# Kernel optimization log

Measured on AMD Instinct MI355X. Metric: run time of the kernel, lower is better.

## Reference

```python
import jax, jax.numpy as jnp
import numpy as np

N_NODES = 50000
N_EDGES = 300000
NODE_DIM = 11
EDGE_DIM = 5
HID = 256
L = 4
G = 1024  # num graphs
BN_EPS = 1e-5


def setup_inputs() -> dict:
    key = jax.random.key(0)
    ks = jax.random.split(key, 24)
    s = 0.05
    inp = {
        "x": jax.random.normal(ks[0], (N_NODES, NODE_DIM), jnp.float32),
        "edge_index": jax.random.randint(ks[1], (2, N_EDGES), 0, N_NODES, jnp.int32),
        "edge_attr": jax.random.normal(ks[2], (N_EDGES, EDGE_DIM), jnp.float32),
        "batch": jnp.sort(jax.random.randint(ks[3], (N_NODES,), 0, G, jnp.int32)),
        # node encoder
        "enc_W": jax.random.normal(ks[4], (NODE_DIM, HID), jnp.float32) * s,
        "enc_b": jnp.zeros((HID,), jnp.float32),
        # per-layer GINE params (stacked over layers)
        "edge_W": jax.random.normal(ks[5], (L, EDGE_DIM, HID), jnp.float32) * s,
        "edge_b": jnp.zeros((L, HID), jnp.float32),
        "mlp_W1": jax.random.normal(ks[6], (L, HID, HID), jnp.float32) * s,
        "mlp_b1": jnp.zeros((L, HID), jnp.float32),
        "mlp_W2": jax.random.normal(ks[7], (L, HID, HID), jnp.float32) * s,
        "mlp_b2": jnp.zeros((L, HID), jnp.float32),
        "bn_g": jnp.ones((L, HID), jnp.float32),
        "bn_b": jnp.zeros((L, HID), jnp.float32),
        # head: 3*HID -> HID -> HID//2 -> 1
        "head_W1": jax.random.normal(ks[8], (3 * HID, HID), jnp.float32) * s,
        "head_b1": jnp.zeros((HID,), jnp.float32),
        "head_W2": jax.random.normal(ks[9], (HID, HID // 2), jnp.float32) * s,
        "head_b2": jnp.zeros((HID // 2,), jnp.float32),
        "head_W3": jax.random.normal(ks[10], (HID // 2, 1), jnp.float32) * s,
        "head_b3": jnp.zeros((1,), jnp.float32),
    }
    return inp


def _forward(x, edge_attr, enc_W, enc_b, edge_W, edge_b, mlp_W1, mlp_b1,
             mlp_W2, mlp_b2, bn_g, bn_b, head_W1, head_b1, head_W2, head_b2,
             head_W3, head_b3, edge_index, batch):
    n = x.shape[0]
    src, dst = edge_index[0], edge_index[1]  # messages flow src(j) -> dst(i)
    h = jax.nn.relu(x @ enc_W + enc_b)  # [N, HID]
    for l in range(L):
        e = edge_attr @ edge_W[l] + edge_b[l]                 # [E, HID]
        msg = jax.nn.relu(h[src] + e)                         # [E, HID]
        aggr = jax.ops.segment_sum(msg, dst, num_segments=n)  # [N, HID]
        z = h + aggr                                          # (1+eps)*h + aggr, eps=0
        z = jax.nn.relu(z @ mlp_W1[l] + mlp_b1[l]) @ mlp_W2[l] + mlp_b2[l]
        # BatchNorm over node dim (batch statistics)
        mu = jnp.mean(z, axis=0)
        var = jnp.var(z, axis=0)
        z = (z - mu) * jax.lax.rsqrt(var + BN_EPS) * bn_g[l] + bn_b[l]
        h = jax.nn.relu(z) + h  # residual
    # mean / add / max pooling per graph
    sums = jax.ops.segment_sum(h, batch, num_segments=G)      # [G, HID]
    cnt = jax.ops.segment_sum(jnp.ones((n, 1), h.dtype), batch, num_segments=G)
    mean = sums / jnp.maximum(cnt, 1.0)
    mx = jax.ops.segment_max(h, batch, num_segments=G)
    g = jnp.concatenate([mean, sums, mx], axis=1)             # [G, 3*HID]
    g = jax.nn.relu(g @ head_W1 + head_b1)
    g = jax.nn.relu(g @ head_W2 + head_b2)
    out = g @ head_W3 + head_b3
    return out.reshape(-1)  # [G]


def reference(x, edge_index, edge_attr, batch, enc_W, enc_b, edge_W, edge_b,
              mlp_W1, mlp_b1, mlp_W2, mlp_b2, bn_g, bn_b, head_W1, head_b1,
              head_W2, head_b2, head_W3, head_b3):
    return _forward(x, edge_attr, enc_W, enc_b, edge_W, edge_b, mlp_W1, mlp_b1,
                    mlp_W2, mlp_b2, bn_g, bn_b, head_W1, head_b1, head_W2,
                    head_b2, head_W3, head_b3, edge_index, batch)
```

## Files before the change

### kernel.cpp

```cpp
#include <hip/hip_runtime.h>

#define N_NODES 50000
#define N_EDGES 300000
#define G_GRAPHS 1024
#define HID 256
#define NLAYERS 4
#define PAD_SLOTS (N_EDGES + 3 * N_NODES + 64)
#define BMT 224

typedef unsigned short ushort_t;
typedef __attribute__((ext_vector_type(8))) short bf16x8;
typedef __attribute__((ext_vector_type(8))) unsigned short u16x8;
typedef __attribute__((ext_vector_type(4))) float f32x4;

__device__ __forceinline__ float bf2f(ushort_t u) {
  unsigned int x = ((unsigned int)u) << 16;
  return __builtin_bit_cast(float, x);
}
__device__ __forceinline__ ushort_t f2bf(float f) {
  unsigned int x = __builtin_bit_cast(unsigned int, f);
  unsigned int lsb = (x >> 16) & 1u;
  x += 0x7fffu + lsb;
  return (ushort_t)(x >> 16);
}

__global__ __launch_bounds__(256) void k_encoder(const float* __restrict__ x,
    const float* __restrict__ W, const float* __restrict__ b,
    ushort_t* __restrict__ h, int n)
{
  int j = threadIdx.x;
  float wcol[11];
#pragma unroll
  for (int k = 0; k < 11; ++k) wcol[k] = W[k * HID + j];
  float bj = b[j];
  __shared__ float xs[8][11];
  int base = blockIdx.x * 8;
  if (j < 88) {
    int r = j / 11, k = j % 11;
    int row = base + r;
    if (row < n) xs[r][k] = x[row * 11 + k];
  }
  __syncthreads();
#pragma unroll
  for (int r = 0; r < 8; ++r) {
    int row = base + r;
    if (row >= n) break;
    float acc = bj;
#pragma unroll
    for (int k = 0; k < 11; ++k) acc += xs[r][k] * wcol[k];
    h[(size_t)row * HID + j] = f2bf(fmaxf(acc, 0.f));
  }
}

__global__ __launch_bounds__(256) void k_hist(const int* __restrict__ dst,
    int* __restrict__ offs, int E)
{
  int e = blockIdx.x * 256 + threadIdx.x;
  if (e < E) atomicAdd(&offs[dst[e]], 1);
}

__global__ __launch_bounds__(1024) void k_scanA(int* __restrict__ offs,
    int* __restrict__ btot, int n)
{
  __shared__ int wsum[16];
  int tid = threadIdx.x, lane = tid & 63, wid = tid >> 6;
  int idx = blockIdx.x * 1024 + tid;
  int cnt = (idx < n) ? offs[idx] : 0;
  int v = (cnt + 3) & ~3;
  int x = v;
#pragma unroll
  for (int off = 1; off < 64; off <<= 1) {
    int t = __shfl_up(x, off);
    if (lane >= off) x += t;
  }
  if (lane == 63) wsum[wid] = x;
  __syncthreads();
  if (wid == 0 && lane < 16) {
    int w = wsum[lane];
#pragma unroll
    for (int off = 1; off < 16; off <<= 1) {
      int t = __shfl_up(w, off);
      if (lane >= off) w += t;
    }
    wsum[lane] = w;
  }
  __syncthreads();
  int wbase = (wid == 0) ? 0 : wsum[wid - 1];
  if (idx < n) offs[idx] = wbase + x - v;
  if (tid == 0) btot[blockIdx.x] = wsum[15];
}

__global__ __launch_bounds__(1024) void k_scanC(int* __restrict__ offs,
    int* __restrict__ pstart, const int* __restrict__ btot, int n)
{
  __shared__ int sbase;
  if (threadIdx.x == 0) {
    int s = 0;
    for (int i = 0; i < (int)blockIdx.x; ++i) s += btot[i];
    sbase = s;
    if (blockIdx.x == gridDim.x - 1) pstart[n] = s + btot[blockIdx.x];
  }
  __syncthreads();
  int idx = blockIdx.x * 1024 + threadIdx.x;
  if (idx < n) {
    int v = offs[idx] + sbase;
    offs[idx] = v;
    pstart[idx] = v;
  }
}

__global__ __launch_bounds__(256) void k_fill(const int* __restrict__ src,
    const int* __restrict__ dst, int* __restrict__ offs,
    int* __restrict__ esrc, ushort_t* __restrict__ eab,
    const float* __restrict__ ea, int E)
{
  int e = blockIdx.x * 256 + threadIdx.x;
  if (e < E) {
    int d = dst[e];
    int p = atomicAdd(&offs[d], 1);
    esrc[p] = src[e];
    const float* ep = ea + (size_t)e * 5;
    ushort4 lo = make_ushort4(f2bf(ep[0]), f2bf(ep[1]), f2bf(ep[2]), f2bf(ep[3]));
    ushort4 hi = make_ushort4(f2bf(ep[4]), (ushort_t)0x3f80u, 0, 0);
    *(ushort4*)&eab[(size_t)p * 8] = lo;
    *(ushort4*)&eab[(size_t)p * 8 + 4] = hi;
  }
}

__global__ __launch_bounds__(256) void k_prep(const float* __restrict__ W1,
    const float* __restrict__ W2, ushort_t* __restrict__ Wt1,
    ushort_t* __restrict__ Wt2)
{
  __shared__ float ld[16][257];
  int mat = blockIdx.y & (NLAYERS - 1);
  int which = blockIdx.y >> 2;
  const float* Wm = (which ? W2 : W1) + (size_t)mat * HID * HID;
  ushort_t* Wtm = (which ? Wt2 : Wt1) + (size_t)mat * HID * HID;
  int k0 = blockIdx.x * 16;
  int tid = threadIdx.x;
#pragma unroll
  for (int i = 0; i < 16; ++i) ld[i][tid] = Wm[(size_t)(k0 + i) * HID + tid];
  __syncthreads();
#pragma unroll
  for (int v = 0; v < 4; ++v) {
    ushort4 u = make_ushort4(f2bf(ld[v*4+0][tid]), f2bf(ld[v*4+1][tid]),
                             f2bf(ld[v*4+2][tid]), f2bf(ld[v*4+3][tid]));
    *(ushort4*)&Wtm[(size_t)tid * HID + k0 + v * 4] = u;
  }
}

__global__ __launch_bounds__(256) void k_prept(const float* __restrict__ W,
    ushort_t* __restrict__ Wt, int K, int N)
{
  int idx = blockIdx.x * 256 + threadIdx.x;
  if (idx >= K * N) return;
  int n = idx / K, k = idx % K;
  Wt[idx] = f2bf(W[(size_t)k * N + n]);
}

__device__ __forceinline__ void edge_step(bf16x8 ev, ushort4 hv,
    const float4& w0, const float4& w1, const float4& w2, const float4& w3,
    const float4& w4, const float4& bi,
    float& ax, float& ay, float& az, float& aw)
{
  float v0 = bf2f((ushort_t)ev[0]), v1 = bf2f((ushort_t)ev[1]),
        v2 = bf2f((ushort_t)ev[2]), v3 = bf2f((ushort_t)ev[3]),
        v4 = bf2f((ushort_t)ev[4]), fl = bf2f((ushort_t)ev[5]);
  float m0 = bi.x, m1 = bi.y, m2 = bi.z, m3 = bi.w;
  m0 = fmaf(v0, w0.x, m0); m1 = fmaf(v0, w0.y, m1);
  m2 = fmaf(v0, w0.z, m2); m3 = fmaf(v0, w0.w, m3);
  m0 = fmaf(v1, w1.x, m0); m1 = fmaf(v1, w1.y, m1);
  m2 = fmaf(v1, w1.z, m2); m3 = fmaf(v1, w1.w, m3);
  m0 = fmaf(v2, w2.x, m0); m1 = fmaf(v2, w2.y, m1);
  m2 = fmaf(v2, w2.z, m2); m3 = fmaf(v2, w2.w, m3);
  m0 = fmaf(v3, w3.x, m0); m1 = fmaf(v3, w3.y, m1);
  m2 = fmaf(v3, w3.z, m2); m3 = fmaf(v3, w3.w, m3);
  m0 = fmaf(v4, w4.x, m0); m1 = fmaf(v4, w4.y, m1);
  m2 = fmaf(v4, w4.z, m2); m3 = fmaf(v4, w4.w, m3);
  m0 += bf2f(hv.x); m1 += bf2f(hv.y); m2 += bf2f(hv.z); m3 += bf2f(hv.w);
  ax = fmaf(fl, fmaxf(m0, 0.f), ax);
  ay = fmaf(fl, fmaxf(m1, 0.f), ay);
  az = fmaf(fl, fmaxf(m2, 0.f), az);
  aw = fmaf(fl, fmaxf(m3, 0.f), aw);
}

__global__ __launch_bounds__(256) void k_gather(const ushort_t* __restrict__ h,
    const int* __restrict__ pstart, const int* __restrict__ esrc,
    const ushort_t* __restrict__ eab, const float* __restrict__ eW,
    const float* __restrict__ eb, ushort_t* __restrict__ zin,
    float* __restrict__ stats, int n)
{
  int tid = threadIdx.x;
  if (blockIdx.x == 0) { stats[tid] = 0.f; stats[HID + tid] = 0.f; }
  int wave = tid >> 6, lane = tid & 63;
  int c4 = lane * 4;
  float4 w0 = *(const float4*)&eW[0 * HID + c4];
  float4 w1 = *(const float4*)&eW[1 * HID + c4];
  float4 w2 = *(const float4*)&eW[2 * HID + c4];
  float4 w3 = *(const float4*)&eW[3 * HID + c4];
  float4 w4 = *(const float4*)&eW[4 * HID + c4];
  float4 bi = *(const float4*)&eb[c4];
  int n0 = (blockIdx.x * 4 + wave) * 4;
  if (n0 >= n) return;
  int e0 = __builtin_amdgcn_readfirstlane(pstart[n0]);
  int e1 = __builtin_amdgcn_readfirstlane(pstart[n0 + 1]);
  int e2 = __builtin_amdgcn_readfirstlane(pstart[n0 + 2]);
  int e3 = __builtin_amdgcn_readfirstlane(pstart[n0 + 3]);
  int e4 = __builtin_amdgcn_readfirstlane(pstart[n0 + 4]);
  float A[4][4];
#pragma unroll
  for (int j = 0; j < 4; ++j) {
    ushort4 hv = *(const ushort4*)&h[(size_t)(n0 + j) * HID + c4];
    A[j][0] = bf2f(hv.x); A[j][1] = bf2f(hv.y);
    A[j][2] = bf2f(hv.z); A[j][3] = bf2f(hv.w);
  }
  int p = e0, pend = e4;
  bf16x8 ec0, ec1, ec2, ec3;
  ushort4 hc0, hc1, hc2, hc3;
  int sn0, sn1, sn2, sn3;
  if (p < pend) {
    int sc0 = esrc[p], sc1 = esrc[p + 1], sc2 = esrc[p + 2], sc3 = esrc[p + 3];
    ec0 = *(const bf16x8*)&eab[(size_t)(p + 0) * 8];
    ec1 = *(const bf16x8*)&eab[(size_t)(p + 1) * 8];
    ec2 = *(const bf16x8*)&eab[(size_t)(p + 2) * 8];
    ec3 = *(const bf16x8*)&eab[(size_t)(p + 3) * 8];
    hc0 = *(const ushort4*)&h[(size_t)sc0 * HID + c4];
    hc1 = *(const ushort4*)&h[(size_t)sc1 * HID + c4];
    hc2 = *(const ushort4*)&h[(size_t)sc2 * HID + c4];
    hc3 = *(const ushort4*)&h[(size_t)sc3 * HID + c4];
    int pn = (p + 4 < pend) ? p + 4 : p;
    sn0 = esrc[pn]; sn1 = esrc[pn + 1]; sn2 = esrc[pn + 2]; sn3 = esrc[pn + 3];
  }
  for (; p < pend; p += 4) {
    int pn = (p + 4 < pend) ? p + 4 : p;
    int pnn = (p + 8 < pend) ? p + 8 : p;
    bf16x8 en0 = *(const bf16x8*)&eab[(size_t)(pn + 0) * 8];
    bf16x8 en1 = *(const bf16x8*)&eab[(size_t)(pn + 1) * 8];
    bf16x8 en2 = *(const bf16x8*)&eab[(size_t)(pn + 2) * 8];
    bf16x8 en3 = *(const bf16x8*)&eab[(size_t)(pn + 3) * 8];
    ushort4 hn0 = *(const ushort4*)&h[(size_t)sn0 * HID + c4];
    ushort4 hn1 = *(const ushort4*)&h[(size_t)sn1 * HID + c4];
    ushort4 hn2 = *(const ushort4*)&h[(size_t)sn2 * HID + c4];
    ushort4 hn3 = *(const ushort4*)&h[(size_t)sn3 * HID + c4];
    int sm0 = esrc[pnn], sm1 = esrc[pnn + 1], sm2 = esrc[pnn + 2], sm3 = esrc[pnn + 3];
    float c0 = 0.f, c1 = 0.f, c2 = 0.f, c3 = 0.f;
    edge_step(ec0, hc0, w0, w1, w2, w3, w4, bi, c0, c1, c2, c3);
    edge_step(ec1, hc1, w0, w1, w2, w3, w4, bi, c0, c1, c2, c3);
    edge_step(ec2, hc2, w0, w1, w2, w3, w4, bi, c0, c1, c2, c3);
    edge_step(ec3, hc3, w0, w1, w2, w3, w4, bi, c0, c1, c2, c3);
    if (p < e1)      { A[0][0] += c0; A[0][1] += c1; A[0][2] += c2; A[0][3] += c3; }
    else if (p < e2) { A[1][0] += c0; A[1][1] += c1; A[1][2] += c2; A[1][3] += c3; }
    else if (p < e3) { A[2][0] += c0; A[2][1] += c1; A[2][2] += c2; A[2][3] += c3; }
    else             { A[3][0] += c0; A[3][1] += c1; A[3][2] += c2; A[3][3] += c3; }
    ec0 = en0; ec1 = en1; ec2 = en2; ec3 = en3;
    hc0 = hn0; hc1 = hn1; hc2 = hn2; hc3 = hn3;
    sn0 = sm0; sn1 = sm1; sn2 = sm2; sn3 = sm3;
  }
#pragma unroll
  for (int j = 0; j < 4; ++j) {
    *(ushort4*)&zin[(size_t)(n0 + j) * HID + c4] =
        make_ushort4(f2bf(A[j][0]), f2bf(A[j][1]), f2bf(A[j][2]), f2bf(A[j][3]));
  }
}

__global__ __launch_bounds__(512, 1) void k_mlp(const ushort_t* __restrict__ A,
    const ushort_t* __restrict__ Wt1, const float* __restrict__ b1,
    const ushort_t* __restrict__ Wt2, const float* __restrict__ b2,
    ushort_t* __restrict__ out, float* __restrict__ stats, int M)
{
  __shared__ alignas(16) ushort_t T[BMT][264];
  int tid = threadIdx.x;
  int wave = tid >> 6, lane = tid & 63;
  int m = lane & 15, quad = lane >> 4;
  int col0 = wave * 32;
  int row0 = blockIdx.x * BMT;

#pragma unroll
  for (int i = 0; i < 14; ++i) {
    int flat = i * 512 + tid;
    int row = flat >> 5, kc = flat & 31;
    int gr = row0 + row; if (gr > M - 1) gr = M - 1;
    u16x8 v = *(const u16x8*)(A + (size_t)gr * HID + kc * 8);
    *(u16x8*)&T[row][kc * 8] = v;
  }
  bf16x8 w1f[2][8];
#pragma unroll
  for (int nt = 0; nt < 2; ++nt)
#pragma unroll
    for (int kt = 0; kt < 8; ++kt)
      w1f[nt][kt] = *(const bf16x8*)(
          Wt1 + (size_t)(col0 + nt * 16 + m) * HID + kt * 32 + quad * 8);
  float bv1[2] = {b1[col0 + m], b1[col0 + 16 + m]};
  float bv2[2] = {b2[col0 + m], b2[col0 + 16 + m]};
  __syncthreads();

  f32x4 acc[14][2];
#pragma unroll
  for (int mt = 0; mt < 14; ++mt) {
    acc[mt][0] = (f32x4){0.f, 0.f, 0.f, 0.f};
    acc[mt][1] = (f32x4){0.f, 0.f, 0.f, 0.f};
    bf16x8 af[8];
#pragma unroll
    for (int kt = 0; kt < 8; ++kt)
      af[kt] = *(const bf16x8*)&T[mt * 16 + m][kt * 32 + quad * 8];
#pragma unroll
    for (int kt = 0; kt < 8; ++kt) {
      acc[mt][0] = __builtin_amdgcn_mfma_f32_16x16x32_bf16(af[kt], w1f[0][kt], acc[mt][0], 0, 0, 0);
      acc[mt][1] = __builtin_amdgcn_mfma_f32_16x16x32_bf16(af[kt], w1f[1][kt], acc[mt][1], 0, 0, 0);
    }
  }
  __syncthreads();

#pragma unroll
  for (int mt = 0; mt < 14; ++mt)
#pragma unroll
    for (int nt = 0; nt < 2; ++nt)
#pragma unroll
      for (int reg = 0; reg < 4; ++reg)
        T[mt * 16 + quad * 4 + reg][col0 + nt * 16 + m] =
            f2bf(fmaxf(acc[mt][nt][reg] + bv1[nt], 0.f));
  bf16x8 w2f[2][8];
#pragma unroll
  for (int nt = 0; nt < 2; ++nt)
#pragma unroll
    for (int kt = 0; kt < 8; ++kt)
      w2f[nt][kt] = *(const bf16x8*)(
          Wt2 + (size_t)(col0 + nt * 16 + m) * HID + kt * 32 + quad * 8);
  __syncthreads();

#pragma unroll
  for (int mt = 0; mt < 14; ++mt) {
    acc[mt][0] = (f32x4){0.f, 0.f, 0.f, 0.f};
    acc[mt][1] = (f32x4){0.f, 0.f, 0.f, 0.f};
    bf16x8 af[8];
#pragma unroll
    for (int kt = 0; kt < 8; ++kt)
      af[kt] = *(const bf16x8*)&T[mt * 16 + m][kt * 32 + quad * 8];
#pragma unroll
    for (int kt = 0; kt < 8; ++kt) {
      acc[mt][0] = __builtin_amdgcn_mfma_f32_16x16x32_bf16(af[kt], w2f[0][kt], acc[mt][0], 0, 0, 0);
      acc[mt][1] = __builtin_amdgcn_mfma_f32_16x16x32_bf16(af[kt], w2f[1][kt], acc[mt][1], 0, 0, 0);
    }
  }

  float csum[2] = {0.f, 0.f}, csq[2] = {0.f, 0.f};
#pragma unroll
  for (int mt = 0; mt < 14; ++mt) {
    if (row0 + mt * 16 < M) {
#pragma unroll
      for (int nt = 0; nt < 2; ++nt) {
#pragma unroll
        for (int reg = 0; reg < 4; ++reg) {
          float o = acc[mt][nt][reg] + bv2[nt];
          out[(size_t)(row0 + mt * 16 + quad * 4 + reg) * HID + col0 + nt * 16 + m] = f2bf(o);
          csum[nt] += o; csq[nt] = fmaf(o, o, csq[nt]);
        }
      }
    }
  }
#pragma unroll
  for (int nt = 0; nt < 2; ++nt) {
    float s = csum[nt], q = csq[nt];
    s += __shfl_xor(s, 16); s += __shfl_xor(s, 32);
    q += __shfl_xor(q, 16); q += __shfl_xor(q, 32);
    if (quad == 0) {
      unsafeAtomicAdd(&stats[col0 + nt * 16 + m], s);
      unsafeAtomicAdd(&stats[HID + col0 + nt * 16 + m], q);
    }
  }
}

__global__ __launch_bounds__(256) void k_bn_apply(const ushort_t* __restrict__ z,
    const float* __restrict__ stats, const float* __restrict__ g,
    const float* __restrict__ b, ushort_t* __restrict__ h, int total4)
{
  int idx = blockIdx.x * 256 + threadIdx.x;
  if (idx >= total4) return;
  int col = (idx & 63) * 4;
  const float inv_n = 1.f / (float)N_NODES;
  float sc[4], sh[4];
#pragma unroll
  for (int c = 0; c < 4; ++c) {
    float mu = stats[col + c] * inv_n;
    float var = stats[HID + col + c] * inv_n - mu * mu;
    float rs = rsqrtf(var + 1e-5f);
    sc[c] = g[col + c] * rs;
    sh[c] = b[col + c] - mu * sc[c];
  }
  ushort4 zv = *(const ushort4*)(z + (size_t)idx * 4);
  ushort4 hv = *(const ushort4*)(h + (size_t)idx * 4);
  float o0 = fmaxf(fmaf(bf2f(zv.x), sc[0], sh[0]), 0.f) + bf2f(hv.x);
  float o1 = fmaxf(fmaf(bf2f(zv.y), sc[1], sh[1]), 0.f) + bf2f(hv.y);
  float o2 = fmaxf(fmaf(bf2f(zv.z), sc[2], sh[2]), 0.f) + bf2f(hv.z);
  float o3 = fmaxf(fmaf(bf2f(zv.w), sc[3], sh[3]), 0.f) + bf2f(hv.w);
  *(ushort4*)(h + (size_t)idx * 4) = make_ushort4(f2bf(o0), f2bf(o1), f2bf(o2), f2bf(o3));
}

__device__ __forceinline__ int lbound(const int* __restrict__ b, int n, int key) {
  int lo = 0, hi = n;
  while (lo < hi) {
    int mid = (lo + hi) >> 1;
    if (b[mid] < key) lo = mid + 1; else hi = mid;
  }
  return lo;
}

__global__ __launch_bounds__(256) void k_pool_bn(const ushort_t* __restrict__ z,
    const float* __restrict__ stats, const float* __restrict__ g_,
    const float* __restrict__ b_, const ushort_t* __restrict__ h,
    const int* __restrict__ batch, ushort_t* __restrict__ gf)
{
  int g = blockIdx.x, j = threadIdx.x;
  const float inv_n = 1.f / (float)N_NODES;
  float mu = stats[j] * inv_n;
  float var = stats[HID + j] * inv_n - mu * mu;
  float rs = rsqrtf(var + 1e-5f);
  float sc = g_[j] * rs;
  float sh = b_[j] - mu * sc;
  int lo = lbound(batch, N_NODES, g);
  int hi = lbound(batch, N_NODES, g + 1);
  float s = 0.f, mx = 0.f;
  for (int i = lo; i < hi; ++i) {
    float zv = bf2f(z[(size_t)i * HID + j]);
    float hv = bf2f(h[(size_t)i * HID + j]);
    float v = fmaxf(fmaf(zv, sc, sh), 0.f) + hv;
    s += v; mx = fmaxf(mx, v);
  }
  float cntv = fmaxf((float)(hi - lo), 1.f);
  size_t base = (size_t)g * 768;
  gf[base + j] = f2bf(s / cntv);
  gf[base + 256 + j] = f2bf(s);
  gf[base + 512 + j] = f2bf(mx);
}

template<int KT, int DO_RELU>
__global__ __launch_bounds__(256, 1) void k_head_gemm(const ushort_t* __restrict__ A,
    const ushort_t* __restrict__ Bt, const float* __restrict__ bias,
    ushort_t* __restrict__ out, int M, int N)
{
  const int K = KT * 32;
  int tid = threadIdx.x;
  int wave = tid >> 6, lane = tid & 63;
  int m = lane & 15, quad = lane >> 4;
  int col = (blockIdx.y * 4 + wave) * 16 + m;
  bf16x8 bfrag[KT];
#pragma unroll
  for (int kt = 0; kt < KT; ++kt)
    bfrag[kt] = *(const bf16x8*)(Bt + (size_t)col * K + kt * 32 + quad * 8);
  float bv = bias[col];
  int ntiles = M >> 4;
  for (int t = blockIdx.x; t < ntiles; t += gridDim.x) {
    const ushort_t* Ap = A + (size_t)(t * 16 + m) * K + quad * 8;
    bf16x8 af[KT];
#pragma unroll
    for (int kt = 0; kt < KT; ++kt) af[kt] = *(const bf16x8*)(Ap + kt * 32);
    f32x4 acc = (f32x4){0.f, 0.f, 0.f, 0.f};
#pragma unroll
    for (int kt = 0; kt < KT; ++kt)
      acc = __builtin_amdgcn_mfma_f32_16x16x32_bf16(af[kt], bfrag[kt], acc, 0, 0, 0);
    int rb = t * 16 + quad * 4;
#pragma unroll
    for (int reg = 0; reg < 4; ++reg) {
      float o = acc[reg] + bv;
      if (DO_RELU) o = fmaxf(o, 0.f);
      out[(size_t)(rb + reg) * N + col] = f2bf(o);
    }
  }
}

__global__ __launch_bounds__(256) void k_head_out(const ushort_t* __restrict__ g2,
    const float* __restrict__ W3, const float* __restrict__ b3,
    float* __restrict__ out)
{
  int wave = threadIdx.x >> 6, lane = threadIdx.x & 63;
  int g = blockIdx.x * 4 + wave;
  ushort2 v = *(const ushort2*)&g2[(size_t)g * 128 + lane * 2];
  float p = bf2f(v.x) * W3[lane * 2] + bf2f(v.y) * W3[lane * 2 + 1];
#pragma unroll
  for (int off = 32; off > 0; off >>= 1) p += __shfl_down(p, off);
  if (lane == 0) out[g] = p + b3[0];
}

extern "C" void kernel_launch(void* const* d_in, const int* in_sizes, int n_in,
                              void* d_out, int out_size, void* d_ws, size_t ws_size,
                              hipStream_t stream)
{
  const float* x     = (const float*)d_in[0];
  const int*   ei    = (const int*)d_in[1];
  const float* ea    = (const float*)d_in[2];
  const int*   batch = (const int*)d_in[3];
  const float* encW  = (const float*)d_in[4];
  const float* encB  = (const float*)d_in[5];
  const float* edgeW = (const float*)d_in[6];
  const float* edgeB = (const float*)d_in[7];
  const float* W1    = (const float*)d_in[8];
  const float* b1    = (const float*)d_in[9];
  const float* W2    = (const float*)d_in[10];
  const float* b2    = (const float*)d_in[11];
  const float* bng   = (const float*)d_in[12];
  const float* bnb   = (const float*)d_in[13];
  const float* hW1   = (const float*)d_in[14];
  const float* hb1   = (const float*)d_in[15];
  const float* hW2   = (const float*)d_in[16];
  const float* hb2   = (const float*)d_in[17];
  const float* hW3   = (const float*)d_in[18];
  const float* hb3   = (const float*)d_in[19];
  float* out = (float*)d_out;

  const size_t NH = (size_t)N_NODES * HID;
  char* base = (char*)d_ws;
  auto alloc = [&](size_t bytes) -> char* {
    char* p = base; base += (bytes + 63) & ~(size_t)63; return p;
  };
  float*    stats = (float*)alloc(512 * 4);
  int*      offs  = (int*)alloc(50001 * 4);
  int*      pstart= (int*)alloc(50001 * 4);
  int*      btot  = (int*)alloc(64 * 4);
  int*      esrc  = (int*)alloc((size_t)PAD_SLOTS * 4);
  ushort_t* eab   = (ushort_t*)alloc((size_t)PAD_SLOTS * 8 * 2);
  ushort_t* Wt1   = (ushort_t*)alloc((size_t)NLAYERS * HID * HID * 2);
  ushort_t* Wt2   = (ushort_t*)alloc((size_t)NLAYERS * HID * HID * 2);
  ushort_t* hW1t  = (ushort_t*)alloc((size_t)768 * 256 * 2);
  ushort_t* hW2t  = (ushort_t*)alloc((size_t)256 * 128 * 2);
  ushort_t* gf    = (ushort_t*)alloc((size_t)G_GRAPHS * 768 * 2);
  ushort_t* g1    = (ushort_t*)alloc((size_t)G_GRAPHS * 256 * 2);
  ushort_t* g2    = (ushort_t*)alloc((size_t)G_GRAPHS * 128 * 2);
  ushort_t* zin   = (ushort_t*)alloc(NH * 2);
  ushort_t* h     = (ushort_t*)alloc(NH * 2);

  const int* src = ei;
  const int* dst = ei + N_EDGES;

  hipMemsetAsync(offs, 0, 50001 * sizeof(int), stream);
  hipMemsetAsync(esrc, 0, (size_t)PAD_SLOTS * 4, stream);
  hipMemsetAsync(eab, 0, (size_t)PAD_SLOTS * 16, stream);
  k_hist<<<(N_EDGES + 255) / 256, 256, 0, stream>>>(dst, offs, N_EDGES);
  const int NSB = (N_NODES + 1023) / 1024;
  k_scanA<<<NSB, 1024, 0, stream>>>(offs, btot, N_NODES);
  k_scanC<<<NSB, 1024, 0, stream>>>(offs, pstart, btot, N_NODES);
  k_fill<<<(N_EDGES + 255) / 256, 256, 0, stream>>>(src, dst, offs, esrc, eab, ea, N_EDGES);
  k_prep<<<dim3(16, 2 * NLAYERS), 256, 0, stream>>>(W1, W2, Wt1, Wt2);
  k_prept<<<(768 * 256 + 255) / 256, 256, 0, stream>>>(hW1, hW1t, 768, 256);
  k_prept<<<(256 * 128 + 255) / 256, 256, 0, stream>>>(hW2, hW2t, 256, 128);

  k_encoder<<<(N_NODES + 7) / 8, 256, 0, stream>>>(x, encW, encB, h, N_NODES);

  const int NB_MLP = (N_NODES + BMT - 1) / BMT;

  for (int l = 0; l < NLAYERS; ++l) {
    k_gather<<<(N_NODES + 15) / 16, 256, 0, stream>>>(
        h, pstart, esrc, eab, edgeW + (size_t)l * 5 * HID, edgeB + (size_t)l * HID,
        zin, stats, N_NODES);
    k_mlp<<<NB_MLP, 512, 0, stream>>>(
        zin, Wt1 + (size_t)l * HID * HID, b1 + (size_t)l * HID,
        Wt2 + (size_t)l * HID * HID, b2 + (size_t)l * HID, zin, stats, N_NODES);
    if (l < NLAYERS - 1) {
      k_bn_apply<<<(N_NODES * HID / 4 + 255) / 256, 256, 0, stream>>>(
          zin, stats, bng + (size_t)l * HID, bnb + (size_t)l * HID, h,
          N_NODES * HID / 4);
    }
  }

  k_pool_bn<<<G_GRAPHS, 256, 0, stream>>>(
      zin, stats, bng + (size_t)(NLAYERS - 1) * HID,
      bnb + (size_t)(NLAYERS - 1) * HID, h, batch, gf);
  k_head_gemm<24, 1><<<dim3(16, 4), 256, 0, stream>>>(gf, hW1t, hb1, g1, G_GRAPHS, 256);
  k_head_gemm<8, 1><<<dim3(16, 2), 256, 0, stream>>>(g1, hW2t, hb2, g2, G_GRAPHS, 128);
  k_head_out<<<G_GRAPHS / 4, 256, 0, stream>>>(g2, hW3, hb3, out);
}
```

Measured before the change: 530.5 us.

## Widen BN apply to 8-wide vectors, unroll pooling loop, merge memsets

The batch-norm apply kernel now processes 8 bf16 values per thread with 16-byte loads and stores instead of 4, which halves the thread count and widens memory transactions. The pooling loop is unrolled by two so more independent loads are in flight per iteration. The two memsets of esrc and eab become one memset over the contiguous span, which assumes the allocator lays the two buffers out adjacently. If they are not adjacent, the merged memset could clear the wrong range.

```diff
diff --git a/kernel.cpp b/kernel.cpp
--- a/kernel.cpp
+++ b/kernel.cpp
@@ -372,28 +372,30 @@
 
 __global__ __launch_bounds__(256) void k_bn_apply(const ushort_t* __restrict__ z,
     const float* __restrict__ stats, const float* __restrict__ g,
-    const float* __restrict__ b, ushort_t* __restrict__ h, int total4)
+    const float* __restrict__ b, ushort_t* __restrict__ h, int total8)
 {
   int idx = blockIdx.x * 256 + threadIdx.x;
-  if (idx >= total4) return;
-  int col = (idx & 63) * 4;
+  if (idx >= total8) return;
+  int col = (idx & 31) * 8;
   const float inv_n = 1.f / (float)N_NODES;
-  float sc[4], sh[4];
-#pragma unroll
-  for (int c = 0; c < 4; ++c) {
+  float sc[8], sh[8];
+#pragma unroll
+  for (int c = 0; c < 8; ++c) {
     float mu = stats[col + c] * inv_n;
     float var = stats[HID + col + c] * inv_n - mu * mu;
     float rs = rsqrtf(var + 1e-5f);
     sc[c] = g[col + c] * rs;
     sh[c] = b[col + c] - mu * sc[c];
   }
-  ushort4 zv = *(const ushort4*)(z + (size_t)idx * 4);
-  ushort4 hv = *(const ushort4*)(h + (size_t)idx * 4);
-  float o0 = fmaxf(fmaf(bf2f(zv.x), sc[0], sh[0]), 0.f) + bf2f(hv.x);
-  float o1 = fmaxf(fmaf(bf2f(zv.y), sc[1], sh[1]), 0.f) + bf2f(hv.y);
-  float o2 = fmaxf(fmaf(bf2f(zv.z), sc[2], sh[2]), 0.f) + bf2f(hv.z);
-  float o3 = fmaxf(fmaf(bf2f(zv.w), sc[3], sh[3]), 0.f) + bf2f(hv.w);
-  *(ushort4*)(h + (size_t)idx * 4) = make_ushort4(f2bf(o0), f2bf(o1), f2bf(o2), f2bf(o3));
+  u16x8 zv = *(const u16x8*)(z + (size_t)idx * 8);
+  u16x8 hv = *(const u16x8*)(h + (size_t)idx * 8);
+  u16x8 o;
+#pragma unroll
+  for (int c = 0; c < 8; ++c) {
+    float v = fmaxf(fmaf(bf2f(zv[c]), sc[c], sh[c]), 0.f) + bf2f(hv[c]);
+    o[c] = f2bf(v);
+  }
+  *(u16x8*)(h + (size_t)idx * 8) = o;
 }
 
 __device__ __forceinline__ int lbound(const int* __restrict__ b, int n, int key) {
@@ -420,7 +422,18 @@
   int lo = lbound(batch, N_NODES, g);
   int hi = lbound(batch, N_NODES, g + 1);
   float s = 0.f, mx = 0.f;
-  for (int i = lo; i < hi; ++i) {
+  int i = lo;
+  for (; i + 1 < hi; i += 2) {
+    float zv0 = bf2f(z[(size_t)i * HID + j]);
+    float hv0 = bf2f(h[(size_t)i * HID + j]);
+    float zv1 = bf2f(z[(size_t)(i + 1) * HID + j]);
+    float hv1 = bf2f(h[(size_t)(i + 1) * HID + j]);
+    float v0 = fmaxf(fmaf(zv0, sc, sh), 0.f) + hv0;
+    float v1 = fmaxf(fmaf(zv1, sc, sh), 0.f) + hv1;
+    s += v0 + v1;
+    mx = fmaxf(mx, fmaxf(v0, v1));
+  }
+  if (i < hi) {
     float zv = bf2f(z[(size_t)i * HID + j]);
     float hv = bf2f(h[(size_t)i * HID + j]);
     float v = fmaxf(fmaf(zv, sc, sh), 0.f) + hv;
@@ -532,8 +545,7 @@
   const int* dst = ei + N_EDGES;
 
   hipMemsetAsync(offs, 0, 50001 * sizeof(int), stream);
-  hipMemsetAsync(esrc, 0, (size_t)PAD_SLOTS * 4, stream);
-  hipMemsetAsync(eab, 0, (size_t)PAD_SLOTS * 16, stream);
+  hipMemsetAsync(esrc, 0, (size_t)((char*)(eab + (size_t)PAD_SLOTS * 8) - (char*)esrc), stream);
   k_hist<<<(N_EDGES + 255) / 256, 256, 0, stream>>>(dst, offs, N_EDGES);
   const int NSB = (N_NODES + 1023) / 1024;
   k_scanA<<<NSB, 1024, 0, stream>>>(offs, btot, N_NODES);
@@ -555,9 +567,9 @@
         zin, Wt1 + (size_t)l * HID * HID, b1 + (size_t)l * HID,
         Wt2 + (size_t)l * HID * HID, b2 + (size_t)l * HID, zin, stats, N_NODES);
     if (l < NLAYERS - 1) {
-      k_bn_apply<<<(N_NODES * HID / 4 + 255) / 256, 256, 0, stream>>>(
+      k_bn_apply<<<(N_NODES * HID / 8 + 255) / 256, 256, 0, stream>>>(
           zin, stats, bng + (size_t)l * HID, bnb + (size_t)l * HID, h,
-          N_NODES * HID / 4);
+          N_NODES * HID / 8);
     }
   }
 
```

Measured after the change: 520.7 us. Within noise of the previous version (-1.8%).
